# Performance work log

Hardware: AMD Instinct MI355X
Metric: run time of the kernel (lower is better)

## Reference

```python
import jax, jax.numpy as jnp
import numpy as np

N_HOS, N_TYPES = 8, 16
N_COMBOS = N_HOS * N_TYPES          # 128
N_STRUCTS = 512
BATCH = 2048
HID = 20
N_ITERS = 60                        # PDHG iterations (fixed, jit-friendly)
CONTROL = 10.0                      # control_strength in the original module


def _spectral_bound(S):
    # ||[S; I]||_2^2 = lambda_max(S^T S + I) via power iteration (S is constant).
    v = jnp.ones((S.shape[1],), S.dtype)
    def pit(v, _):
        u = S.T @ (S @ v) + v
        return u / jnp.linalg.norm(u), None
    v, _ = jax.lax.scan(pit, v, None, length=30)
    return jnp.sqrt(v @ (S.T @ (S @ v) + v))


def _solve_lp(S, b, z):
    """Batched solve of: max 1^T x - CONTROL*||x - z||_2  s.t. x >= 0, S x <= b.
    Chambolle-Pock PDHG with K = [S; -I], f(x) = -1^T x + CONTROL*||x - z||.
    S: [m, n]; b: [B, m]; z: [B, n] -> x: [B, n].
    """
    B, m = b.shape
    n = z.shape[1]
    L = _spectral_bound(S)
    tau = 0.9 / L
    sig = 0.9 / L
    w = jnp.ones((n,), z.dtype)     # LP objective weights (module uses ones)

    x = jnp.maximum(z, 0.0)
    xb = x
    lam1 = jnp.zeros((B, m), z.dtype)   # duals for S x <= b
    lam2 = jnp.zeros((B, n), z.dtype)   # duals for x >= 0 (lam2 <= 0 form)

    def step(carry, _):
        x, xb, lam1, lam2 = carry
        # dual ascent: prox of conjugates of the constraint indicators
        u1 = lam1 + sig * (xb @ S.T)                 # [B, m]
        lam1 = jnp.maximum(u1 - sig * b, 0.0)
        lam2 = jnp.minimum(lam2 + sig * xb, 0.0)
        # primal: prox of tau*(-w^T x + CONTROL*||x - z||): block soft-threshold
        v = x - tau * (lam1 @ S + lam2)
        u = v + tau * w - z
        nrm = jnp.linalg.norm(u, axis=1, keepdims=True)
        scale = jnp.maximum(0.0, 1.0 - tau * CONTROL / jnp.maximum(nrm, 1e-12))
        x_new = z + scale * u
        xb = 2.0 * x_new - x
        return (x_new, xb, lam1, lam2), None

    (x, _, _, _), _ = jax.lax.scan(step, (x, xb, lam1, lam2), None, length=N_ITERS)
    return x


def _mlp(Xf, W1, b1, W2, b2, W3, b3, W4, b4):
    h = jnp.tanh(Xf @ W1 + b1)
    h = jnp.tanh(h @ W2 + b2)
    h = jnp.tanh(h @ W3 + b3)
    return h @ W4 + b4


def setup_inputs() -> dict:
    key = jax.random.key(0)
    ks = jax.random.split(key, 10)
    X = jax.random.uniform(ks[0], (BATCH, N_HOS, N_TYPES), jnp.float32)
    # 0/1 cycle-incidence matrix, ~4 nonzeros per column (cycles of length ~4)
    S = jax.random.bernoulli(ks[1], 4.0 / N_COMBOS, (N_COMBOS, N_STRUCTS)).astype(jnp.float32)
    def lin(k, fi, fo):
        return jax.random.normal(k, (fi, fo), jnp.float32) / jnp.sqrt(fi)
    W1 = lin(ks[2], N_COMBOS, HID); b1 = jnp.zeros((HID,), jnp.float32)
    W2 = lin(ks[3], HID, HID);      b2 = jnp.zeros((HID,), jnp.float32)
    W3 = lin(ks[4], HID, HID);      b3 = jnp.zeros((HID,), jnp.float32)
    W4 = lin(ks[5], HID, N_STRUCTS); b4 = jnp.zeros((N_STRUCTS,), jnp.float32)
    return {"X": X, "W1": W1, "b1": b1, "W2": W2, "b2": b2, "W3": W3,
            "b3": b3, "W4": W4, "b4": b4, "S": S, "batch_size": BATCH}


def reference(X, W1, b1, W2, b2, W3, b3, W4, b4, S, batch_size):
    Xf = X.reshape(batch_size, N_COMBOS)       # bids, also the LP rhs b
    z = _mlp(Xf, W1, b1, W2, b2, W3, b3, W4, b4)   # [B, n_structures]
    return _solve_lp(S, Xf, z)                 # allocation x1 [B, n_structures]
```

## Files before the change

kernel.cpp:

```cpp
#include <hip/hip_runtime.h>


#define NC    128
#define NS    512
#define BATCH 2048
#define HID   20

typedef unsigned int  uint;
typedef unsigned short ushort;
typedef float v2f __attribute__((ext_vector_type(2)));


template <int CTRL, int RMASK = 0xf>
__device__ __forceinline__ float dppadd(float s) {
    return s + __builtin_bit_cast(float,
        __builtin_amdgcn_update_dpp(0, __builtin_bit_cast(int, s), CTRL, RMASK, 0xf, true));
}
__device__ __forceinline__ float quad_sum(float s) {
    s = dppadd<0xB1>(s);
    s = dppadd<0x4E>(s);
    return s;
}
__device__ __forceinline__ float wave_sum_bcast(float x) {
    float s = x;
    s = dppadd<0x111>(s);
    s = dppadd<0x112>(s);
    s = dppadd<0x114>(s);
    s = dppadd<0x118>(s);
    s = dppadd<0x142, 0xa>(s);
    s = dppadd<0x143, 0xc>(s);
    return __builtin_bit_cast(float, __builtin_amdgcn_readlane(__builtin_bit_cast(int, s), 63));
}
__device__ __forceinline__ v2f vfma(v2f a, v2f b, v2f c) { return __builtin_elementwise_fma(a, b, c); }
__device__ __forceinline__ v2f vmax0(v2f a) { const v2f z = {0.f, 0.f}; return __builtin_elementwise_max(a, z); }
__device__ __forceinline__ v2f vmin0(v2f a) { const v2f z = {0.f, 0.f}; return __builtin_elementwise_min(a, z); }

__global__ __launch_bounds__(512) void prep_scan(
    const float* __restrict__ S, uint* __restrict__ colmask_g, uint* __restrict__ rowbits_g)
{
    __shared__ uint mcol[NS];
    const int t = threadIdx.x, g = blockIdx.x;
    float vals[32];
#pragma unroll
    for (int j = 0; j < 32; ++j) vals[j] = S[(g * 32 + j) * NS + t];
    uint m = 0;
#pragma unroll
    for (int j = 0; j < 32; ++j) if (vals[j] != 0.0f) m |= (1u << j);
    mcol[t] = m;
    colmask_g[t * 4 + g] = m;
    __syncthreads();
    const int j = t >> 4, w = t & 15;
    uint val = 0;
#pragma unroll
    for (int c = 0; c < 32; ++c)
        val |= (((mcol[w * 32 + c] >> j) & 1u) << c);
    rowbits_g[(g * 32 + j) * 16 + w] = val;
}

__global__ __launch_bounds__(512) void prep_finish(
    const uint* __restrict__ colmask_g, const uint* __restrict__ rowbits_g,
    float* __restrict__ tau_ws,
    uint* __restrict__ col_meta, uint* __restrict__ col_cnt_g,
    uint* __restrict__ row_meta, uint* __restrict__ row_cnt_g)
{
    __shared__ ushort clist[NS][16];
    __shared__ ushort rql[NS][10];
    __shared__ int    ccnt_l[NS];
    __shared__ int    rcnt_l[NS];
    __shared__ float  u_lds[NS + 1];
    __shared__ float  sv_lds[NC];
    __shared__ float  red_pi[32];
    const int t = threadIdx.x;

    uint cm[4];
    { const uint4 c4 = *(const uint4*)&colmask_g[t * 4];
      cm[0] = c4.x; cm[1] = c4.y; cm[2] = c4.z; cm[3] = c4.w; }
    {
        int cc = 0;
#pragma unroll
        for (int g = 0; g < 4; ++g) {
            uint m = cm[g];
            while (m) {
                const int b = __ffs(m) - 1; m &= m - 1;
                if (cc < 16) clist[t][cc] = (ushort)((g * 32 + b) * 8);
                ++cc;
            }
        }
        if (cc > 16) cc = 16;
        const int cc2 = (cc + 1) & ~1;
        for (int k = cc; k < 16; ++k) clist[t][k] = (ushort)(NC * 8);
        ccnt_l[t] = cc2;
    }
    if (t < NC) {
#pragma unroll
        for (int q = 0; q < 4; ++q)
            for (int p = 0; p < 10; ++p) rql[t * 4 + q][p] = (ushort)(NS * 16);
        uint rb[16];
        { const uint4 a = *(const uint4*)&rowbits_g[t * 16];
          const uint4 b = *(const uint4*)&rowbits_g[t * 16 + 4];
          const uint4 c = *(const uint4*)&rowbits_g[t * 16 + 8];
          const uint4 d = *(const uint4*)&rowbits_g[t * 16 + 12];
          rb[0]=a.x; rb[1]=a.y; rb[2]=a.z;  rb[3]=a.w;  rb[4]=b.x;  rb[5]=b.y;  rb[6]=b.z;  rb[7]=b.w;
          rb[8]=c.x; rb[9]=c.y; rb[10]=c.z; rb[11]=c.w; rb[12]=d.x; rb[13]=d.y; rb[14]=d.z; rb[15]=d.w; }
        int e = 0;
#pragma unroll
        for (int w = 0; w < 16; ++w) {
            uint m = rb[w];
            while (m) {
                const int b = __ffs(m) - 1; m &= m - 1;
                const int q = e & 3, p = e >> 2;
                if (p < 10) rql[t * 4 + q][p] = (ushort)((w * 32 + b) * 16);
                ++e;
            }
        }
#pragma unroll
        for (int q = 0; q < 4; ++q) {
            int n = (e - q + 3) >> 2;
            if (n < 0) n = 0;
            if (n > 10) n = 10;
            rcnt_l[t * 4 + q] = (n + 1) & ~1;
        }
    }
    if (t == 0) u_lds[NS] = 0.0f;
    if (t < 32) red_pi[t] = 0.0f;
    u_lds[t] = 1.0f;
    __syncthreads();

    {
        col_cnt_g[t] = (uint)ccnt_l[t];
#pragma unroll
        for (int k = 0; k < 16; ++k) col_meta[t * 16 + k] = (uint)clist[t][k];
        row_cnt_g[t] = (uint)rcnt_l[t];
#pragma unroll
        for (int k = 0; k < 12; ++k)
            row_meta[t * 12 + k] = (k < 10) ? (uint)rql[t][k] : (uint)(NS * 16);
    }

    const int rcn = rcnt_l[t];
    float u_loc = 1.0f;
    for (int it = 0; it <= 30; ++it) {
        const float inv = it ? rsqrtf(red_pi[it - 1]) : 1.0f;
        float s = 0.0f;
        for (int k = 0; k < rcn; ++k) {
            const uint a = rql[t][k];
            s += *(const float*)((const char*)u_lds + (a >> 2));
        }
        s = quad_sum(s * inv);
        if ((t & 3) == 3) sv_lds[t >> 2] = s;
        __syncthreads();
        const float vt = u_loc * inv;
        float w = vt;
#pragma unroll
        for (int g = 0; g < 4; ++g) {
            uint m = cm[g];
            while (m) { const int b = __ffs(m) - 1; m &= m - 1; w += sv_lds[g * 32 + b]; }
        }
        float p = (it < 30) ? w * w : w * vt;
        p = wave_sum_bcast(p);
        if ((t & 63) == 0) atomicAdd(&red_pi[it], p);
        u_lds[t] = w;
        u_loc = w;
        __syncthreads();
    }
    if (t == 0) tau_ws[0] = 0.9f / sqrtf(red_pi[30]);
}

__global__ __launch_bounds__(512, 8) void solve_kernel(
    const float* __restrict__ X,
    const float* __restrict__ W1, const float* __restrict__ b1,
    const float* __restrict__ W2, const float* __restrict__ b2,
    const float* __restrict__ W3, const float* __restrict__ b3,
    const float* __restrict__ W4, const float* __restrict__ b4,
    const float* __restrict__ tau_ws,
    const uint* __restrict__ col_meta, const uint* __restrict__ col_cnt_g,
    const uint* __restrict__ row_meta, const uint* __restrict__ row_cnt_g,
    float* __restrict__ out)
{
    __shared__ alignas(16) float4 ab_lds[NS + 1];
    __shared__ alignas(16) float2 lam1_lds[NC + 1];
    __shared__ alignas(16) float  red[61][2];
    __shared__ alignas(16) float2 b_lds[NC];
    __shared__ float ha[2][HID], hb[2][HID];

    const int t  = threadIdx.x;
    const int r0 = blockIdx.x * 2, r1 = r0 + 1;

    uint4 cA, cB, cC, cD, rA, rB, rC;
    { const uint4* g = (const uint4*)&col_meta[t * 16];
      cA = g[0]; cB = g[1]; cC = g[2]; cD = g[3]; }
    { const uint4* g = (const uint4*)&row_meta[t * 12];
      rA = g[0]; rB = g[1]; rC = g[2]; }
    int ccv = (int)col_cnt_g[t];
    int rcv = (int)row_cnt_g[t];

    if (t == 0) { ab_lds[NS] = make_float4(0,0,0,0); lam1_lds[NC] = make_float2(0,0); }
    if (t < 122) ((float*)red)[t] = (t >= 120) ? 1e38f : 0.0f;
    if (t < NC) b_lds[t] = make_float2(X[r0 * NC + t], X[r1 * NC + t]);

#pragma unroll
    for (int off = 32; off; off >>= 1) {
        ccv = max(ccv, __shfl_xor(ccv, off));
        rcv = max(rcv, __shfl_xor(rcv, off));
    }
    const int cmax = __builtin_amdgcn_readfirstlane(ccv);
    const int rmax = __builtin_amdgcn_readfirstlane(rcv);
    __syncthreads();

    if (t < 2 * HID) {
        const int rr = t >= HID, tt = t - rr * HID;
        float s = b1[tt];
        for (int k = 0; k < NC; ++k)
            s = fmaf(rr ? b_lds[k].y : b_lds[k].x, W1[k * HID + tt], s);
        ha[rr][tt] = tanhf(s);
    }
    __syncthreads();
    if (t < 2 * HID) {
        const int rr = t >= HID, tt = t - rr * HID;
        float s = b2[tt];
        for (int k = 0; k < HID; ++k) s = fmaf(ha[rr][k], W2[k * HID + tt], s);
        hb[rr][tt] = tanhf(s);
    }
    __syncthreads();
    if (t < 2 * HID) {
        const int rr = t >= HID, tt = t - rr * HID;
        float s = b3[tt];
        for (int k = 0; k < HID; ++k) s = fmaf(hb[rr][k], W3[k * HID + tt], s);
        ha[rr][tt] = tanhf(s);
    }
    __syncthreads();
    float z0 = b4[t], z1 = z0;
    for (int h = 0; h < HID; ++h) {
        const float w = W4[h * NS + t];
        z0 = fmaf(ha[0][h], w, z0);
        z1 = fmaf(ha[1][h], w, z1);
    }

    const float tau = tau_ws[0];
    const float c10 = 10.0f * tau;
    const v2f tauv = {tau, tau};
    const v2f sigv = tauv;
    const int r = t >> 2, q = t & 3;
    const v2f bb = {b_lds[r].x, b_lds[r].y};

    const v2f z  = {z0, z1};
    const v2f z2 = z + z;
    v2f x  = vmax0(z);
    v2f u  = x - z;
    v2f A  = z2 - x;
    v2f Bv = u + u;
    v2f l1 = {0.f, 0.f};
    v2f l2 = {0.f, 0.f};
    ((v2f*)&ab_lds[t])[0] = A;
    ((v2f*)&ab_lds[t])[1] = Bv;
    __syncthreads();

    const char* abB = (const char*)ab_lds;
    const char* lmB = (const char*)lam1_lds;
    int prev = 60;
    for (int it = 0; it < 60; ++it) {
        const float2 rr2 = *(const float2*)red[prev];
        const v2f sc = {fmaxf(0.f, 1.f - c10 * rsqrtf(rr2.x)),
                        fmaxf(0.f, 1.f - c10 * rsqrtf(rr2.y))};
        x = vfma(sc, u, z);
        const v2f xb = vfma(sc, Bv, A);
        l2 = vmin0(vfma(sigv, xb, l2));
        v2f gA = {0.f, 0.f}, gB = {0.f, 0.f};
#define RG(O1, O2) { const float4 g1 = *(const float4*)(abB + (O1));           \
                     const float4 g2 = *(const float4*)(abB + (O2));           \
                     gA += (v2f){g1.x, g1.y}; gB += (v2f){g1.z, g1.w};         \
                     gA += (v2f){g2.x, g2.y}; gB += (v2f){g2.z, g2.w}; }
        RG(rA.x, rA.y)
        RG(rA.z, rA.w)
        if (rmax > 4)  { RG(rB.x, rB.y) }
        if (rmax > 6)  { RG(rB.z, rB.w) }
        if (rmax > 8)  { RG(rC.x, rC.y) }
#undef RG
        const v2f gs = vfma(sc, gB, gA);
        const v2f sv = {quad_sum(gs.x), quad_sum(gs.y)};
        l1 = vmax0(vfma(sigv, sv - bb, l1));
        if (q == 3) lam1_lds[r] = make_float2(l1.x, l1.y);
        __syncthreads();
        v2f s2 = {0.f, 0.f};
#define CG(O1, O2) { s2 += *(const v2f*)(lmB + (O1));                          \
                     s2 += *(const v2f*)(lmB + (O2)); }
        CG(cA.x, cA.y)
        CG(cA.z, cA.w)
        if (cmax > 4)  { CG(cB.x, cB.y) }
        if (cmax > 6)  { CG(cB.z, cB.w) }
        if (cmax > 8)  { CG(cC.x, cC.y) }
        if (cmax > 10) { CG(cC.z, cC.w) }
        if (cmax > 12) { CG(cD.x, cD.y) }
        if (cmax > 14) { CG(cD.z, cD.w) }
#undef CG
        const v2f v = x - tauv * (s2 + l2);
        u  = (v + tauv) - z;
        A  = z2 - x;
        Bv = u + u;
        ((v2f*)&ab_lds[t])[0] = A;
        ((v2f*)&ab_lds[t])[1] = Bv;
        const v2f p = u * u;
        const float p0 = wave_sum_bcast(p.x);
        const float p1 = wave_sum_bcast(p.y);
        if ((t & 63) == 0) { atomicAdd(&red[it][0], p0); atomicAdd(&red[it][1], p1); }
        prev = it;
        __syncthreads();
    }
    const float2 rr2 = *(const float2*)red[59];
    const v2f sc = {fmaxf(0.f, 1.f - c10 * rsqrtf(rr2.x)),
                    fmaxf(0.f, 1.f - c10 * rsqrtf(rr2.y))};
    const v2f xf = vfma(sc, u, z);
    out[r0 * NS + t] = xf.x;
    out[r1 * NS + t] = xf.y;
}

extern "C" void kernel_launch(void* const* d_in, const int* in_sizes, int n_in,
                              void* d_out, int out_size, void* d_ws, size_t ws_size,
                              hipStream_t stream)
{
    const float* X  = (const float*)d_in[0];
    const float* W1 = (const float*)d_in[1];
    const float* b1 = (const float*)d_in[2];
    const float* W2 = (const float*)d_in[3];
    const float* b2 = (const float*)d_in[4];
    const float* W3 = (const float*)d_in[5];
    const float* b3 = (const float*)d_in[6];
    const float* W4 = (const float*)d_in[7];
    const float* b4 = (const float*)d_in[8];
    const float* S  = (const float*)d_in[9];
    float* out = (float*)d_out;

    char* ws = (char*)d_ws;
    float* tau_ws    = (float*)(ws + 0);
    uint*  colmask_g = (uint*)(ws + 64);
    uint*  rowbits_g = (uint*)(ws + 8256);
    uint*  col_meta  = (uint*)(ws + 16448);
    uint*  col_cnt_g = (uint*)(ws + 49216);
    uint*  row_meta  = (uint*)(ws + 51264);
    uint*  row_cnt_g = (uint*)(ws + 75840);

    prep_scan<<<4, 512, 0, stream>>>(S, colmask_g, rowbits_g);
    prep_finish<<<1, 512, 0, stream>>>(colmask_g, rowbits_g, tau_ws,
                                       col_meta, col_cnt_g, row_meta, row_cnt_g);
    solve_kernel<<<BATCH / 2, 512, 0, stream>>>(X, W1, b1, W2, b2, W3, b3, W4, b4,
                                                tau_ws, col_meta, col_cnt_g,
                                                row_meta, row_cnt_g, out);
}
```

Before: 279.8 us.

## Add third barrier per PDHG iteration to gather xb rows from float2 LDS

The old loop deferred the norm-scale by storing two vectors (A, B) per column in a float4 LDS array and reconstructing xb during the row gather. It used atomics into a per-iteration reduction table. The new loop adds a barrier after the wave-partial norm write, reads the eight partials from fixed slots, and computes xb directly. Only a float2 per column is stored, so the row gather reads half the LDS bytes and the offsets are rescaled. The cost is a third __syncthreads per iteration, and the uniform wave-max loop bounds become per-thread nested branches on the count, which may diverge.

Result: no change. 280.1 us (+0.1%).

```diff
diff --git a/kernel.cpp b/kernel.cpp
--- a/kernel.cpp
+++ b/kernel.cpp
@@ -94,7 +94,7 @@
     if (t < NC) {
 #pragma unroll
         for (int q = 0; q < 4; ++q)
-            for (int p = 0; p < 10; ++p) rql[t * 4 + q][p] = (ushort)(NS * 16);
+            for (int p = 0; p < 10; ++p) rql[t * 4 + q][p] = (ushort)(NS * 8);
         uint rb[16];
         { const uint4 a = *(const uint4*)&rowbits_g[t * 16];
           const uint4 b = *(const uint4*)&rowbits_g[t * 16 + 4];
@@ -109,7 +109,7 @@
             while (m) {
                 const int b = __ffs(m) - 1; m &= m - 1;
                 const int q = e & 3, p = e >> 2;
-                if (p < 10) rql[t * 4 + q][p] = (ushort)((w * 32 + b) * 16);
+                if (p < 10) rql[t * 4 + q][p] = (ushort)((w * 32 + b) * 8);
                 ++e;
             }
         }
@@ -133,7 +133,7 @@
         row_cnt_g[t] = (uint)rcnt_l[t];
 #pragma unroll
         for (int k = 0; k < 12; ++k)
-            row_meta[t * 12 + k] = (k < 10) ? (uint)rql[t][k] : (uint)(NS * 16);
+            row_meta[t * 12 + k] = (k < 10) ? (uint)rql[t][k] : (uint)(NS * 8);
     }
 
     const int rcn = rcnt_l[t];
@@ -143,7 +143,7 @@
         float s = 0.0f;
         for (int k = 0; k < rcn; ++k) {
             const uint a = rql[t][k];
-            s += *(const float*)((const char*)u_lds + (a >> 2));
+            s += *(const float*)((const char*)u_lds + (a >> 1));
         }
         s = quad_sum(s * inv);
         if ((t & 3) == 3) sv_lds[t >> 2] = s;
@@ -176,9 +176,9 @@
     const uint* __restrict__ row_meta, const uint* __restrict__ row_cnt_g,
     float* __restrict__ out)
 {
-    __shared__ alignas(16) float4 ab_lds[NS + 1];
+    __shared__ alignas(16) float2 xb_lds[NS + 1];
     __shared__ alignas(16) float2 lam1_lds[NC + 1];
-    __shared__ alignas(16) float  red[61][2];
+    __shared__ alignas(16) float2 redslot[8];
     __shared__ alignas(16) float2 b_lds[NC];
     __shared__ float ha[2][HID], hb[2][HID];
 
@@ -190,20 +190,11 @@
       cA = g[0]; cB = g[1]; cC = g[2]; cD = g[3]; }
     { const uint4* g = (const uint4*)&row_meta[t * 12];
       rA = g[0]; rB = g[1]; rC = g[2]; }
-    int ccv = (int)col_cnt_g[t];
-    int rcv = (int)row_cnt_g[t];
-
-    if (t == 0) { ab_lds[NS] = make_float4(0,0,0,0); lam1_lds[NC] = make_float2(0,0); }
-    if (t < 122) ((float*)red)[t] = (t >= 120) ? 1e38f : 0.0f;
+    const int ccn = (int)col_cnt_g[t];
+    const int rcn = (int)row_cnt_g[t];
+
+    if (t == 0) { xb_lds[NS] = make_float2(0.f, 0.f); lam1_lds[NC] = make_float2(0.f, 0.f); }
     if (t < NC) b_lds[t] = make_float2(X[r0 * NC + t], X[r1 * NC + t]);
-
-#pragma unroll
-    for (int off = 32; off; off >>= 1) {
-        ccv = max(ccv, __shfl_xor(ccv, off));
-        rcv = max(rcv, __shfl_xor(rcv, off));
-    }
-    const int cmax = __builtin_amdgcn_readfirstlane(ccv);
-    const int rmax = __builtin_amdgcn_readfirstlane(rcv);
     __syncthreads();
 
     if (t < 2 * HID) {
@@ -242,75 +233,96 @@
     const int r = t >> 2, q = t & 3;
     const v2f bb = {b_lds[r].x, b_lds[r].y};
 
-    const v2f z  = {z0, z1};
-    const v2f z2 = z + z;
+    const v2f z = {z0, z1};
     v2f x  = vmax0(z);
-    v2f u  = x - z;
-    v2f A  = z2 - x;
-    v2f Bv = u + u;
+    v2f xb = x;
+    v2f u  = {0.f, 0.f};
     v2f l1 = {0.f, 0.f};
-    v2f l2 = {0.f, 0.f};
-    ((v2f*)&ab_lds[t])[0] = A;
-    ((v2f*)&ab_lds[t])[1] = Bv;
-    __syncthreads();
-
-    const char* abB = (const char*)ab_lds;
+    v2f l2 = vmin0(sigv * xb);
+    xb_lds[t] = make_float2(xb.x, xb.y);
+    __syncthreads();
+
+    const char* xbB = (const char*)xb_lds;
     const char* lmB = (const char*)lam1_lds;
-    int prev = 60;
     for (int it = 0; it < 60; ++it) {
-        const float2 rr2 = *(const float2*)red[prev];
-        const v2f sc = {fmaxf(0.f, 1.f - c10 * rsqrtf(rr2.x)),
-                        fmaxf(0.f, 1.f - c10 * rsqrtf(rr2.y))};
-        x = vfma(sc, u, z);
-        const v2f xb = vfma(sc, Bv, A);
-        l2 = vmin0(vfma(sigv, xb, l2));
-        v2f gA = {0.f, 0.f}, gB = {0.f, 0.f};
-#define RG(O1, O2) { const float4 g1 = *(const float4*)(abB + (O1));           \
-                     const float4 g2 = *(const float4*)(abB + (O2));           \
-                     gA += (v2f){g1.x, g1.y}; gB += (v2f){g1.z, g1.w};         \
-                     gA += (v2f){g2.x, g2.y}; gB += (v2f){g2.z, g2.w}; }
-        RG(rA.x, rA.y)
-        RG(rA.z, rA.w)
-        if (rmax > 4)  { RG(rB.x, rB.y) }
-        if (rmax > 6)  { RG(rB.z, rB.w) }
-        if (rmax > 8)  { RG(rC.x, rC.y) }
-#undef RG
-        const v2f gs = vfma(sc, gB, gA);
-        const v2f sv = {quad_sum(gs.x), quad_sum(gs.y)};
-        l1 = vmax0(vfma(sigv, sv - bb, l1));
+        v2f s = {0.f, 0.f};
+        s += *(const v2f*)(xbB + rA.x);
+        s += *(const v2f*)(xbB + rA.y);
+        if (rcn > 2) {
+            s += *(const v2f*)(xbB + rA.z);
+            s += *(const v2f*)(xbB + rA.w);
+            if (rcn > 4) {
+                s += *(const v2f*)(xbB + rB.x);
+                s += *(const v2f*)(xbB + rB.y);
+                if (rcn > 6) {
+                    s += *(const v2f*)(xbB + rB.z);
+                    s += *(const v2f*)(xbB + rB.w);
+                    if (rcn > 8) {
+                        s += *(const v2f*)(xbB + rC.x);
+                        s += *(const v2f*)(xbB + rC.y);
+                    }
+                }
+            }
+        }
+        const v2f sq = {quad_sum(s.x), quad_sum(s.y)};
+        l1 = vmax0(vfma(sigv, sq - bb, l1));
         if (q == 3) lam1_lds[r] = make_float2(l1.x, l1.y);
         __syncthreads();
         v2f s2 = {0.f, 0.f};
-#define CG(O1, O2) { s2 += *(const v2f*)(lmB + (O1));                          \
-                     s2 += *(const v2f*)(lmB + (O2)); }
-        CG(cA.x, cA.y)
-        CG(cA.z, cA.w)
-        if (cmax > 4)  { CG(cB.x, cB.y) }
-        if (cmax > 6)  { CG(cB.z, cB.w) }
-        if (cmax > 8)  { CG(cC.x, cC.y) }
-        if (cmax > 10) { CG(cC.z, cC.w) }
-        if (cmax > 12) { CG(cD.x, cD.y) }
-        if (cmax > 14) { CG(cD.z, cD.w) }
-#undef CG
+        s2 += *(const v2f*)(lmB + cA.x);
+        s2 += *(const v2f*)(lmB + cA.y);
+        if (ccn > 2) {
+            s2 += *(const v2f*)(lmB + cA.z);
+            s2 += *(const v2f*)(lmB + cA.w);
+            if (ccn > 4) {
+                s2 += *(const v2f*)(lmB + cB.x);
+                s2 += *(const v2f*)(lmB + cB.y);
+                if (ccn > 6) {
+                    s2 += *(const v2f*)(lmB + cB.z);
+                    s2 += *(const v2f*)(lmB + cB.w);
+                    if (ccn > 8) {
+                        s2 += *(const v2f*)(lmB + cC.x);
+                        s2 += *(const v2f*)(lmB + cC.y);
+                        if (ccn > 10) {
+                            s2 += *(const v2f*)(lmB + cC.z);
+                            s2 += *(const v2f*)(lmB + cC.w);
+                            if (ccn > 12) {
+                                s2 += *(const v2f*)(lmB + cD.x);
+                                s2 += *(const v2f*)(lmB + cD.y);
+                                if (ccn > 14) {
+                                    s2 += *(const v2f*)(lmB + cD.z);
+                                    s2 += *(const v2f*)(lmB + cD.w);
+                                }
+                            }
+                        }
+                    }
+                }
+            }
+        }
         const v2f v = x - tauv * (s2 + l2);
-        u  = (v + tauv) - z;
-        A  = z2 - x;
-        Bv = u + u;
-        ((v2f*)&ab_lds[t])[0] = A;
-        ((v2f*)&ab_lds[t])[1] = Bv;
+        u = (v + tauv) - z;
         const v2f p = u * u;
         const float p0 = wave_sum_bcast(p.x);
         const float p1 = wave_sum_bcast(p.y);
-        if ((t & 63) == 0) { atomicAdd(&red[it][0], p0); atomicAdd(&red[it][1], p1); }
-        prev = it;
-        __syncthreads();
-    }
-    const float2 rr2 = *(const float2*)red[59];
-    const v2f sc = {fmaxf(0.f, 1.f - c10 * rsqrtf(rr2.x)),
-                    fmaxf(0.f, 1.f - c10 * rsqrtf(rr2.y))};
-    const v2f xf = vfma(sc, u, z);
-    out[r0 * NS + t] = xf.x;
-    out[r1 * NS + t] = xf.y;
+        if ((t & 63) == 0) redslot[t >> 6] = make_float2(p0, p1);
+        __syncthreads();
+        const float4* rs = (const float4*)redslot;
+        const float4 Ra = rs[0], Rb = rs[1], Rc = rs[2], Rd = rs[3];
+        const v2f tot = (((v2f){Ra.x, Ra.y} + (v2f){Ra.z, Ra.w}) +
+                         ((v2f){Rb.x, Rb.y} + (v2f){Rb.z, Rb.w})) +
+                        (((v2f){Rc.x, Rc.y} + (v2f){Rc.z, Rc.w}) +
+                         ((v2f){Rd.x, Rd.y} + (v2f){Rd.z, Rd.w}));
+        const v2f sc = {fmaxf(0.f, 1.f - c10 * rsqrtf(tot.x)),
+                        fmaxf(0.f, 1.f - c10 * rsqrtf(tot.y))};
+        const v2f xn = vfma(sc, u, z);
+        xb = (xn + xn) - x;
+        x  = xn;
+        l2 = vmin0(vfma(sigv, xb, l2));
+        xb_lds[t] = make_float2(xb.x, xb.y);
+        __syncthreads();
+    }
+    out[r0 * NS + t] = x.x;
+    out[r1 * NS + t] = x.y;
 }
 
 extern "C" void kernel_launch(void* const* d_in, const int* in_sizes, int n_in,
```
